# Kernel tuning notes

Hardware: AMD Instinct MI355X
Metric: run time of the kernel (lower is better)

## Reference

```python
import jax, jax.numpy as jnp
import numpy as np
import math

B, CK, T, H, W = 4, 64, 8, 30, 54
N, CV = 8, 512

def setup_inputs() -> dict:
    key = jax.random.key(0)
    k1, k2, k3, k4 = jax.random.split(key, 4)
    mem_keys = jax.random.normal(k1, (B, CK, T, H, W), dtype=jnp.float32)
    mem_values = jax.random.normal(k2, (N, CV, T, H, W), dtype=jnp.float32)
    qk = jax.random.normal(k3, (B, CK, H, W), dtype=jnp.float32)
    broadcast_map = jax.random.randint(k4, (N,), 0, B, dtype=jnp.int64)
    return {"mem_keys": mem_keys, "mem_values": mem_values, "qk": qk,
            "broadcast_map": broadcast_map}

def reference(mem_keys, mem_values, qk, broadcast_map):
    # STCNModel.read_memory
    Bq, CKq, Tq, Hq, Wq = mem_keys.shape
    mk = mem_keys.reshape(Bq, CKq, Tq * Hq * Wq)      # [B, CK, THW]
    q = qk.reshape(Bq, CKq, Hq * Wq)                   # [B, CK, HW]
    a_sq = jnp.sum(mk * mk, axis=1)[:, :, None]        # [B, THW, 1]
    ab = jnp.einsum('bct,bcq->btq', mk, q)             # [B, THW, HW]
    frame_affinity = (2.0 * ab - a_sq) / math.sqrt(CKq)
    # softmax over memory dim (axis=1)
    frame_affinity = jax.nn.softmax(frame_affinity, axis=1)
    obj_affinity = frame_affinity[broadcast_map]       # [N, THW, HW]
    Nn, CVv = mem_values.shape[0], mem_values.shape[1]
    mo = mem_values.reshape(Nn, CVv, Tq * Hq * Wq)     # [N, CV, THW]
    obj_read = jnp.einsum('nct,ntq->ncq', mo, obj_affinity)
    return obj_read.reshape(Nn, CVv, Hq, Wq)
```

## Files before the change

kernel.cpp:

```cpp
#include <hip/hip_runtime.h>
#include <hip/hip_bf16.h>

#define CKDIM 64
#define THW   12960
#define HWDIM 1620
#define NOBJ  8
#define CVAL  512
#define NB    4
#define NSTEP 405
#define NJT   13
#define NCHS  8
#define NCHP  4
#define PCH   16
#define S2F   0.3606737602222409f

using bf16x8 = __attribute__((ext_vector_type(8))) short;
using f32x4  = __attribute__((ext_vector_type(4))) float;

__device__ __forceinline__ unsigned cvtpk(float lo, float hi) {
    unsigned r;
    asm("v_cvt_pk_bf16_f32 %0, %1, %2" : "=v"(r) : "v"(lo), "v"(hi));
    return r;
}
__device__ __forceinline__ unsigned short bf_rne(float x) {
    unsigned u = __float_as_uint(x);
    u += 0x7FFFu + ((u >> 16) & 1u);
    return (unsigned short)(u >> 16);
}
__device__ __forceinline__ float fexp2(float x) {
#if __has_builtin(__builtin_amdgcn_exp2f)
    return __builtin_amdgcn_exp2f(x);
#else
    return __expf(x * 0.69314718055994531f);
#endif
}

__global__ void stcn_ksq_kernel(const float* __restrict__ mk, float* __restrict__ k8l) {
    int t = blockIdx.x * 256 + threadIdx.x;
    if (t >= THW) return;
    int b = blockIdx.y;
    const float* p = mk + (size_t)b * CKDIM * THW + t;
    float s = 0.f;
#pragma unroll
    for (int c = 0; c < CKDIM; ++c) { float v = p[(size_t)c * THW]; s = fmaf(v, v, s); }
    k8l[b * THW + t] = s * (0.125f * 1.44269504088896341f);
}

__global__ __launch_bounds__(512)
void stcn_ktr_kernel(const float* __restrict__ mk, unsigned short* __restrict__ kbt) {
    __shared__ unsigned short L[64][72];
    const int tid = threadIdx.x, b = blockIdx.y, t0 = blockIdx.x * 64;
#pragma unroll
    for (int it = 0; it < 8; ++it) {
        int idx = tid + 512 * it;
        int tt = idx & 63, c = idx >> 6;
        int t = t0 + tt;
        float v = (t < THW) ? mk[((size_t)b * CKDIM + c) * THW + t] : 0.f;
        L[tt][c] = bf_rne(v);
    }
    __syncthreads();
    int tt = tid >> 3, cq = tid & 7;
    int t = t0 + tt;
    if (t < THW) {
        uint4 o = *(const uint4*)&L[tt][8 * cq];
        *(uint4*)(kbt + ((size_t)b * THW + t) * CKDIM + 8 * cq) = o;
    }
}

__global__ void stcn_vcvt_kernel(const float* __restrict__ mv, unsigned short* __restrict__ mvb) {
    size_t i = ((size_t)blockIdx.x * 256 + threadIdx.x) * 8;
    if (i >= (size_t)NOBJ * CVAL * THW) return;
    float4 v0 = *(const float4*)(mv + i);
    float4 v1 = *(const float4*)(mv + i + 4);
    uint4 o;
    o.x = cvtpk(v0.x, v0.y); o.y = cvtpk(v0.z, v0.w);
    o.z = cvtpk(v1.x, v1.y); o.w = cvtpk(v1.z, v1.w);
    *(uint4*)(mvb + i) = o;
}

template <int MODE, bool VB16, bool KB16>
__global__ __launch_bounds__(512, (MODE == 1) ? 4 : 1)
void stcn_aff_kernel(const float* __restrict__ mk, const unsigned short* __restrict__ kbt,
                     const float* __restrict__ qk, const float* __restrict__ k8l,
                     float* __restrict__ mpart, float* __restrict__ lpart,
                     const float* __restrict__ mv, const unsigned short* __restrict__ mvb,
                     const int* __restrict__ bmap, float* __restrict__ out)
{
    constexpr int SMEM_BYTES = (MODE == 0) ? 36864 : 45312;
    __shared__ __align__(16) unsigned char smem[SMEM_BYTES];
    unsigned short* KtP   = (unsigned short*)smem;
    float*          k8tP  = (float*)(smem + 9216);
    unsigned short* PtP   = (unsigned short*)(smem + 9472);
    unsigned short* VtP   = (unsigned short*)(smem + 23808);
    float*          mjsP  = (float*)(smem + 44288);
    float*          iljsP = (float*)(smem + 44800);
    unsigned short* QtP   = (unsigned short*)smem;

    const int tid  = threadIdx.x;
    const int w    = tid >> 6;
    const int lane = tid & 63;
    const int g    = lane >> 4;
    const int lr   = lane & 15;

    int b, n = 0, jt, kc, cb = 0;
    if (MODE == 0) { b = blockIdx.y; jt = blockIdx.x >> 3; kc = blockIdx.x & 7; }
    else {
        n = blockIdx.y; jt = blockIdx.x >> 3; kc = (blockIdx.x >> 1) & 3; cb = blockIdx.x & 1;
        b = bmap[n];
    }
    const int jbase = jt * 128;
    const int cbase = cb * 256;

#pragma unroll
    for (int it = 0; it < 8; ++it) {
        int idx = tid + 512 * it;
        int j = idx & 127, cp = idx >> 7;
        int jg = jbase + j;
        float q0 = 0.f, q1 = 0.f;
        if (jg < HWDIM) {
            const float* qp = qk + ((size_t)b * CKDIM + 2 * cp) * HWDIM + jg;
            q0 = qp[0]; q1 = qp[HWDIM];
        }
        unsigned wh = cvtpk(q0, q1);
        float r0 = q0 - __uint_as_float(wh << 16);
        float r1 = q1 - __uint_as_float(wh & 0xFFFF0000u);
        *(unsigned*)&QtP[(0 * 128 + j) * 72 + 2 * cp] = wh;
        *(unsigned*)&QtP[(1 * 128 + j) * 72 + 2 * cp] = cvtpk(r0, r1);
    }
    __syncthreads();
    bf16x8 bqh[2], bql[2];
#pragma unroll
    for (int s = 0; s < 2; ++s) {
        bqh[s] = *(const bf16x8*)&QtP[(0 * 128 + w * 16 + lr) * 72 + 32 * s + 8 * g];
        bql[s] = *(const bf16x8*)&QtP[(1 * 128 + w * 16 + lr) * 72 + 32 * s + 8 * g];
    }
    __syncthreads();

    auto stageK_loads = [&](int st, uint2& k16, float2* kvf) {
        if constexpr (KB16) {
            int tt = tid >> 4, cq = tid & 15;
            k16 = *(const uint2*)(kbt + ((size_t)b * THW + st * 32 + tt) * CKDIM + 4 * cq);
        } else {
#pragma unroll
            for (int it = 0; it < 2; ++it) {
                int idx = tid + 512 * it;
                int tt = idx & 31, cp = idx >> 5;
                const float* kp = mk + ((size_t)b * CKDIM + 2 * cp) * THW + st * 32 + tt;
                kvf[it].x = kp[0];
                kvf[it].y = kp[THW];
            }
        }
    };
    auto stageK_write = [&](int buf, uint2 k16, const float2* kvf) {
        if constexpr (KB16) {
            int tt = tid >> 4, cq = tid & 15;
            *(uint2*)&KtP[(buf * 32 + tt) * 72 + 4 * cq] = k16;
        } else {
#pragma unroll
            for (int it = 0; it < 2; ++it) {
                int idx = tid + 512 * it;
                int tt = idx & 31, cp = idx >> 5;
                *(unsigned*)&KtP[(buf * 32 + tt) * 72 + 2 * cp] = cvtpk(kvf[it].x, kvf[it].y);
            }
        }
    };

    int s0, s1;
    if (MODE == 0) { s0 = (NSTEP * kc) / NCHS; s1 = (NSTEP * (kc + 1)) / NCHS; }
    else           { s0 = (NSTEP * kc) / NCHP; s1 = (NSTEP * (kc + 1)) / NCHP; }

    if (MODE == 1 && tid < 128) {
        int jg = jbase + tid;
        float m = 0.f, l = 0.f;
        if (jg < HWDIM) {
            m = -1e30f;
#pragma unroll
            for (int c = 0; c < NCHS; ++c) {
                float mc = mpart[(b * NCHS + c) * HWDIM + jg];
                float lc = lpart[(b * NCHS + c) * HWDIM + jg];
                float mn = fmaxf(m, mc);
                l = l * fexp2(m - mn) + lc * fexp2(mc - mn);
                m = mn;
            }
        }
        mjsP[tid]  = m;
        iljsP[tid] = (l > 0.f) ? 1.f / l : 0.f;
    }
    {
        uint2 k16; float2 kvf[2];
        stageK_loads(s0, k16, kvf);
        stageK_write(0, k16, kvf);
        if (tid < 32) k8tP[tid] = k8l[b * THW + s0 * 32 + tid];
    }
    __syncthreads();

    float mv_j = 0.f, il_j = 0.f;
    if (MODE == 1) { mv_j = mjsP[w * 16 + lr]; il_j = iljsP[w * 16 + lr]; }

    float m_run = -1e30f, l_run = 0.f;
    f32x4 zz = {0.f, 0.f, 0.f, 0.f};
    f32x4 acc[4][4];
    if (MODE == 1)
#pragma unroll
        for (int i = 0; i < 4; ++i)
#pragma unroll
            for (int j = 0; j < 4; ++j) acc[i][j] = zz;

    const int wc = w >> 1, wj = w & 1;
    const int vc = tid >> 1, vth = tid & 1;

    int cur = 0;
    for (int st = s0; st < s1; ++st) {
        const int t0 = st * 32;
        const bool nxt = (st + 1 < s1);

        uint4 vw0 = {0,0,0,0}, vw1 = {0,0,0,0};
        if (MODE == 1) {
            if (VB16) {
                const unsigned short* vp = mvb + ((size_t)n * CVAL + cbase + vc) * THW + t0 + vth * 16;
                vw0 = *(const uint4*)vp;
                vw1 = *(const uint4*)(vp + 8);
            } else {
                const float* vp = mv + ((size_t)n * CVAL + cbase + vc) * THW + t0 + vth * 16;
                float4 f0 = *(const float4*)vp;
                float4 f1 = *(const float4*)(vp + 4);
                float4 f2 = *(const float4*)(vp + 8);
                float4 f3 = *(const float4*)(vp + 12);
                vw0 = make_uint4(cvtpk(f0.x,f0.y), cvtpk(f0.z,f0.w), cvtpk(f1.x,f1.y), cvtpk(f1.z,f1.w));
                vw1 = make_uint4(cvtpk(f2.x,f2.y), cvtpk(f2.z,f2.w), cvtpk(f3.x,f3.y), cvtpk(f3.z,f3.w));
            }
        }
        uint2 k16; float2 kvf[2];
        float k8next = 0.f;
        if (nxt) {
            stageK_loads(st + 1, k16, kvf);
            if (tid < 32) k8next = k8l[b * THW + (st + 1) * 32 + tid];
        }
        bf16x8 ak0[2], ak1[2];
#pragma unroll
        for (int s = 0; s < 2; ++s) {
            ak0[s] = *(const bf16x8*)&KtP[(cur * 32 + lr) * 72 + 32 * s + 8 * g];
            ak1[s] = *(const bf16x8*)&KtP[(cur * 32 + 16 + lr) * 72 + 32 * s + 8 * g];
        }
        f32x4 k80 = *(const f32x4*)&k8tP[cur * 32 + 4 * g];
        f32x4 k81 = *(const f32x4*)&k8tP[cur * 32 + 16 + 4 * g];
        f32x4 ab0 = zz, ab1 = zz;
#pragma unroll
        for (int s = 0; s < 2; ++s) {
            ab0 = __builtin_amdgcn_mfma_f32_16x16x32_bf16(ak0[s], bqh[s], ab0, 0, 0, 0);
            ab0 = __builtin_amdgcn_mfma_f32_16x16x32_bf16(ak0[s], bql[s], ab0, 0, 0, 0);
            ab1 = __builtin_amdgcn_mfma_f32_16x16x32_bf16(ak1[s], bqh[s], ab1, 0, 0, 0);
            ab1 = __builtin_amdgcn_mfma_f32_16x16x32_bf16(ak1[s], bql[s], ab1, 0, 0, 0);
        }
        if (nxt) {
            stageK_write(cur ^ 1, k16, kvf);
            if (tid < 32) k8tP[(cur ^ 1) * 32 + tid] = k8next;
        }

        if (MODE == 0) {
            float L0[4], L1[4], tmax = -1e30f;
#pragma unroll
            for (int r = 0; r < 4; ++r) {
                L0[r] = fmaf(ab0[r], S2F, -k80[r]); tmax = fmaxf(tmax, L0[r]);
                L1[r] = fmaf(ab1[r], S2F, -k81[r]); tmax = fmaxf(tmax, L1[r]);
            }
            float ps = 0.f;
#pragma unroll
            for (int r = 0; r < 4; ++r)
                ps += fexp2(L0[r] - tmax) + fexp2(L1[r] - tmax);
            float mn = fmaxf(m_run, tmax);
            l_run = l_run * fexp2(m_run - mn) + ps * fexp2(tmax - mn);
            m_run = mn;
            __syncthreads();
        } else {
            float p0[4], p1[4];
#pragma unroll
            for (int r = 0; r < 4; ++r) {
                p0[r] = fexp2(fmaf(ab0[r], S2F, -k80[r]) - mv_j) * il_j;
                p1[r] = fexp2(fmaf(ab1[r], S2F, -k81[r]) - mv_j) * il_j;
            }
            __syncthreads();
            {
                int jl = w * 16 + lr;
                *(uint2*)&PtP[jl * 56 + 4 * g]      = make_uint2(cvtpk(p0[0], p0[1]), cvtpk(p0[2], p0[3]));
                *(uint2*)&PtP[jl * 56 + 16 + 4 * g] = make_uint2(cvtpk(p1[0], p1[1]), cvtpk(p1[2], p1[3]));
                *(uint4*)&VtP[vc * 40 + vth * 16]     = vw0;
                *(uint4*)&VtP[vc * 40 + vth * 16 + 8] = vw1;
            }
            __syncthreads();
            bf16x8 bp[4];
#pragma unroll
            for (int jf = 0; jf < 4; ++jf)
                bp[jf] = *(const bf16x8*)&PtP[(wj * 64 + jf * 16 + lr) * 56 + 8 * g];
#pragma unroll
            for (int cf = 0; cf < 4; ++cf) {
                bf16x8 av = *(const bf16x8*)&VtP[(wc * 64 + cf * 16 + lr) * 40 + 8 * g];
#pragma unroll
                for (int jf = 0; jf < 4; ++jf)
                    acc[cf][jf] = __builtin_amdgcn_mfma_f32_16x16x32_bf16(av, bp[jf], acc[cf][jf], 0, 0, 0);
            }
        }
        cur ^= 1;
    }

    if (MODE == 0) {
#pragma unroll
        for (int off = 16; off < 64; off <<= 1) {
            float mo = __shfl_xor(m_run, off, 64);
            float lo = __shfl_xor(l_run, off, 64);
            float mn = fmaxf(m_run, mo);
            l_run = l_run * fexp2(m_run - mn) + lo * fexp2(mo - mn);
            m_run = mn;
        }
        int jg = jbase + w * 16 + lr;
        if (g == 0 && jg < HWDIM) {
            mpart[(b * NCHS + kc) * HWDIM + jg] = m_run;
            lpart[(b * NCHS + kc) * HWDIM + jg] = l_run;
        }
    } else {
#pragma unroll
        for (int cf = 0; cf < 4; ++cf) {
#pragma unroll
            for (int jf = 0; jf < 4; ++jf) {
                int jg = jbase + wj * 64 + jf * 16 + lr;
                if (jg < HWDIM) {
                    int c = cbase + wc * 64 + cf * 16 + 4 * g;
                    float* op = out + ((size_t)n * CVAL + c) * HWDIM + jg;
#pragma unroll
                    for (int r = 0; r < 4; ++r)
                        atomicAdd(op + (size_t)r * HWDIM, acc[cf][jf][r]);
                }
            }
        }
    }
}

__global__ __launch_bounds__(512)
void stcn_pwrite_kernel(const unsigned short* __restrict__ kbt,
                        const float* __restrict__ qk, const float* __restrict__ k8l,
                        const float* __restrict__ mpart, const float* __restrict__ lpart,
                        unsigned short* __restrict__ Pws, int bbase)
{
    __shared__ __align__(16) unsigned char smem[36864];
    unsigned short* KtP   = (unsigned short*)smem;
    float*          k8tP  = (float*)(smem + 9216);
    unsigned short* PtP   = (unsigned short*)(smem + 9472);
    float*          mjsP  = (float*)(smem + 23808);
    float*          iljsP = (float*)(smem + 24320);
    unsigned short* QtP   = (unsigned short*)smem;

    const int tid  = threadIdx.x;
    const int w    = tid >> 6;
    const int lane = tid & 63;
    const int g    = lane >> 4;
    const int lr   = lane & 15;

    const int bb = blockIdx.y;
    const int b  = bbase + bb;
    const int jt = blockIdx.x >> 4, kc = blockIdx.x & 15;
    const int jbase = jt * 128;

#pragma unroll
    for (int it = 0; it < 8; ++it) {
        int idx = tid + 512 * it;
        int j = idx & 127, cp = idx >> 7;
        int jg = jbase + j;
        float q0 = 0.f, q1 = 0.f;
        if (jg < HWDIM) {
            const float* qp = qk + ((size_t)b * CKDIM + 2 * cp) * HWDIM + jg;
            q0 = qp[0]; q1 = qp[HWDIM];
        }
        unsigned wh = cvtpk(q0, q1);
        float r0 = q0 - __uint_as_float(wh << 16);
        float r1 = q1 - __uint_as_float(wh & 0xFFFF0000u);
        *(unsigned*)&QtP[(0 * 128 + j) * 72 + 2 * cp] = wh;
        *(unsigned*)&QtP[(1 * 128 + j) * 72 + 2 * cp] = cvtpk(r0, r1);
    }
    __syncthreads();
    bf16x8 bqh[2], bql[2];
#pragma unroll
    for (int s = 0; s < 2; ++s) {
        bqh[s] = *(const bf16x8*)&QtP[(0 * 128 + w * 16 + lr) * 72 + 32 * s + 8 * g];
        bql[s] = *(const bf16x8*)&QtP[(1 * 128 + w * 16 + lr) * 72 + 32 * s + 8 * g];
    }
    __syncthreads();

    const int s0 = (NSTEP * kc) / PCH, s1 = (NSTEP * (kc + 1)) / PCH;

    if (tid < 128) {
        int jg = jbase + tid;
        float m = 0.f, l = 0.f;
        if (jg < HWDIM) {
            m = -1e30f;
#pragma unroll
            for (int c = 0; c < NCHS; ++c) {
                float mc = mpart[(b * NCHS + c) * HWDIM + jg];
                float lc = lpart[(b * NCHS + c) * HWDIM + jg];
                float mn = fmaxf(m, mc);
                l = l * fexp2(m - mn) + lc * fexp2(mc - mn);
                m = mn;
            }
        }
        mjsP[tid]  = m;
        iljsP[tid] = (l > 0.f) ? 1.f / l : 0.f;
    }
    {
        int tt = tid >> 4, cq = tid & 15;
        uint2 k16 = *(const uint2*)(kbt + ((size_t)b * THW + s0 * 32 + tt) * CKDIM + 4 * cq);
        *(uint2*)&KtP[tt * 72 + 4 * cq] = k16;
        if (tid < 32) k8tP[tid] = k8l[b * THW + s0 * 32 + tid];
    }
    __syncthreads();

    const float mv_j = mjsP[w * 16 + lr], il_j = iljsP[w * 16 + lr];
    f32x4 zz = {0.f, 0.f, 0.f, 0.f};

    int cur = 0;
    for (int st = s0; st < s1; ++st) {
        const int t0 = st * 32;
        const bool nxt = (st + 1 < s1);
        uint2 k16;
        float k8next = 0.f;
        const int tt = tid >> 4, cq = tid & 15;
        if (nxt) {
            k16 = *(const uint2*)(kbt + ((size_t)b * THW + (st + 1) * 32 + tt) * CKDIM + 4 * cq);
            if (tid < 32) k8next = k8l[b * THW + (st + 1) * 32 + tid];
        }
        bf16x8 ak0[2], ak1[2];
#pragma unroll
        for (int s = 0; s < 2; ++s) {
            ak0[s] = *(const bf16x8*)&KtP[(cur * 32 + lr) * 72 + 32 * s + 8 * g];
            ak1[s] = *(const bf16x8*)&KtP[(cur * 32 + 16 + lr) * 72 + 32 * s + 8 * g];
        }
        f32x4 k80 = *(const f32x4*)&k8tP[cur * 32 + 4 * g];
        f32x4 k81 = *(const f32x4*)&k8tP[cur * 32 + 16 + 4 * g];
        f32x4 ab0 = zz, ab1 = zz;
#pragma unroll
        for (int s = 0; s < 2; ++s) {
            ab0 = __builtin_amdgcn_mfma_f32_16x16x32_bf16(ak0[s], bqh[s], ab0, 0, 0, 0);
            ab0 = __builtin_amdgcn_mfma_f32_16x16x32_bf16(ak0[s], bql[s], ab0, 0, 0, 0);
            ab1 = __builtin_amdgcn_mfma_f32_16x16x32_bf16(ak1[s], bqh[s], ab1, 0, 0, 0);
            ab1 = __builtin_amdgcn_mfma_f32_16x16x32_bf16(ak1[s], bql[s], ab1, 0, 0, 0);
        }
        if (nxt) {
            *(uint2*)&KtP[((cur ^ 1) * 32 + tt) * 72 + 4 * cq] = k16;
            if (tid < 32) k8tP[(cur ^ 1) * 32 + tid] = k8next;
        }
        float p0[4], p1[4];
#pragma unroll
        for (int r = 0; r < 4; ++r) {
            p0[r] = fexp2(fmaf(ab0[r], S2F, -k80[r]) - mv_j) * il_j;
            p1[r] = fexp2(fmaf(ab1[r], S2F, -k81[r]) - mv_j) * il_j;
        }
        __syncthreads();
        {
            int jl = w * 16 + lr;
            *(uint2*)&PtP[jl * 56 + 4 * g]      = make_uint2(cvtpk(p0[0], p0[1]), cvtpk(p0[2], p0[3]));
            *(uint2*)&PtP[jl * 56 + 16 + 4 * g] = make_uint2(cvtpk(p1[0], p1[1]), cvtpk(p1[2], p1[3]));
        }
        __syncthreads();
        {
            int jr = tid >> 2, qq = tid & 3;
            int jg = jbase + jr;
            if (jg < HWDIM)
                *(uint4*)(Pws + ((size_t)bb * HWDIM + jg) * THW + t0 + qq * 8) =
                    *(const uint4*)&PtP[jr * 56 + qq * 8];
        }
        cur ^= 1;
    }
}

template <bool FULLP>
__global__ __launch_bounds__(512, 4)
void stcn_gemm2_kernel(const unsigned short* __restrict__ mvb,
                       const unsigned short* __restrict__ Pws,
                       const int* __restrict__ bmap, float* __restrict__ out, int phase)
{
    __shared__ __align__(16) unsigned short Av[2][256 * 40];
    __shared__ __align__(16) unsigned short Bv[2][128 * 40];

    const int n = blockIdx.y;
    const int b = bmap[n];
    int bslot;
    if constexpr (FULLP) { bslot = b; }
    else { if ((b >> 1) != phase) return; bslot = b & 1; }

    const int x    = blockIdx.x;
    const int ks   = x & 3;
    const int rest = x >> 2;
    const int jn   = rest % NJT;
    const int cm   = rest / NJT;
    const int jbase = jn * 128, cbase = cm * 256;

    const int tid = threadIdx.x, w = tid >> 6, lane = tid & 63, g = lane >> 4, lr = lane & 15;
    const int wc = w >> 1, wj = w & 1;

    const int arow = tid >> 1, at = (tid & 1) * 16;
    const int brow = tid >> 2, bt = (tid & 3) * 8;
    const unsigned short* vsrc = mvb + ((size_t)n * CVAL + cbase + arow) * THW + at;
    const int jrow = jbase + brow;
    const bool jok = jrow < HWDIM;
    const unsigned short* psrc = Pws + ((size_t)bslot * HWDIM + (jok ? jrow : 0)) * THW + bt;

    const int s0 = (NSTEP * ks) / 4, s1 = (NSTEP * (ks + 1)) / 4;

    f32x4 zz = {0.f, 0.f, 0.f, 0.f};
    f32x4 acc[4][4];
#pragma unroll
    for (int i = 0; i < 4; ++i)
#pragma unroll
        for (int j = 0; j < 4; ++j) acc[i][j] = zz;

    const uint4 zq = make_uint4(0, 0, 0, 0);
    {
        uint4 ta0 = *(const uint4*)(vsrc + (size_t)s0 * 32);
        uint4 ta1 = *(const uint4*)(vsrc + (size_t)s0 * 32 + 8);
        uint4 tb0 = jok ? *(const uint4*)(psrc + (size_t)s0 * 32) : zq;
        *(uint4*)&Av[0][arow * 40 + at]     = ta0;
        *(uint4*)&Av[0][arow * 40 + at + 8] = ta1;
        *(uint4*)&Bv[0][brow * 40 + bt]     = tb0;
    }
    uint4 nA0 = *(const uint4*)(vsrc + (size_t)(s0 + 1) * 32);
    uint4 nA1 = *(const uint4*)(vsrc + (size_t)(s0 + 1) * 32 + 8);
    uint4 nB0 = jok ? *(const uint4*)(psrc + (size_t)(s0 + 1) * 32) : zq;
    __syncthreads();

    int cur = 0;
    for (int st = s0; st < s1; ++st) {
        const bool h1 = (st + 1 < s1), h2 = (st + 2 < s1);
        uint4 fA0, fA1, fB0;
        if (h2) {
            fA0 = *(const uint4*)(vsrc + (size_t)(st + 2) * 32);
            fA1 = *(const uint4*)(vsrc + (size_t)(st + 2) * 32 + 8);
            fB0 = jok ? *(const uint4*)(psrc + (size_t)(st + 2) * 32) : zq;
        }
        bf16x8 bp[4];
#pragma unroll
        for (int jf = 0; jf < 4; ++jf)
            bp[jf] = *(const bf16x8*)&Bv[cur][(wj * 64 + jf * 16 + lr) * 40 + 8 * g];
        if (h1) {
            *(uint4*)&Av[cur ^ 1][arow * 40 + at]     = nA0;
            *(uint4*)&Av[cur ^ 1][arow * 40 + at + 8] = nA1;
            *(uint4*)&Bv[cur ^ 1][brow * 40 + bt]     = nB0;
        }
#pragma unroll
        for (int cf = 0; cf < 4; ++cf) {
            bf16x8 av = *(const bf16x8*)&Av[cur][(wc * 64 + cf * 16 + lr) * 40 + 8 * g];
#pragma unroll
            for (int jf = 0; jf < 4; ++jf)
                acc[cf][jf] = __builtin_amdgcn_mfma_f32_16x16x32_bf16(av, bp[jf], acc[cf][jf], 0, 0, 0);
        }
        __syncthreads();
        if (h2) { nA0 = fA0; nA1 = fA1; nB0 = fB0; }
        cur ^= 1;
    }

#pragma unroll
    for (int cf = 0; cf < 4; ++cf)
#pragma unroll
        for (int jf = 0; jf < 4; ++jf) {
            int jg = jbase + wj * 64 + jf * 16 + lr;
            if (jg < HWDIM) {
                int c = cbase + wc * 64 + cf * 16 + 4 * g;
                float* op = out + ((size_t)n * CVAL + c) * HWDIM + jg;
#pragma unroll
                for (int r = 0; r < 4; ++r)
                    atomicAdd(op + (size_t)r * HWDIM, acc[cf][jf][r]);
            }
        }
}

extern "C" void kernel_launch(void* const* d_in, const int* in_sizes, int n_in,
                              void* d_out, int out_size, void* d_ws, size_t ws_size,
                              hipStream_t stream) {
    (void)in_sizes; (void)n_in;
    const float* mk   = (const float*)d_in[0];
    const float* mv   = (const float*)d_in[1];
    const float* qkp  = (const float*)d_in[2];
    const int*   bmap = (const int*)d_in[3];
    float* out = (float*)d_out;

    float* k8l   = (float*)d_ws;
    float* mpart = k8l + NB * THW;
    float* lpart = mpart + NB * NCHS * HWDIM;
    unsigned short* mvb = (unsigned short*)(lpart + NB * NCHS * HWDIM);
    unsigned short* kbt = mvb + (size_t)NOBJ * CVAL * THW;
    unsigned short* Pws = kbt + (size_t)NB * THW * CKDIM;

    size_t base_bytes = (size_t)(NB * THW + 2 * NB * NCHS * HWDIM) * 4;
    size_t need_vb  = base_bytes + (size_t)NOBJ * CVAL * THW * 2;
    size_t need_kbt = need_vb + (size_t)NB * THW * CKDIM * 2;
    size_t need_P2  = need_kbt + (size_t)2 * HWDIM * THW * 2;
    size_t need_P4  = need_kbt + (size_t)4 * HWDIM * THW * 2;
    bool use_vb16 = (ws_size >= need_vb);
    bool use_kbt  = (ws_size >= need_kbt);
    bool use_P2   = (ws_size >= need_P2);
    bool use_P4   = (ws_size >= need_P4);

    hipMemsetAsync(d_out, 0, (size_t)out_size * sizeof(float), stream);
    stcn_ksq_kernel<<<dim3((THW + 255) / 256, NB), 256, 0, stream>>>(mk, k8l);
    if (use_kbt)
        stcn_ktr_kernel<<<dim3((THW + 63) / 64, NB), 512, 0, stream>>>(mk, kbt);
    if (use_vb16) {
        size_t nthreads = (size_t)NOBJ * CVAL * THW / 8;
        stcn_vcvt_kernel<<<(unsigned)((nthreads + 255) / 256), 256, 0, stream>>>(mv, mvb);
    }

    if (use_kbt)
        stcn_aff_kernel<0, false, true><<<dim3(NJT * NCHS, NB), 512, 0, stream>>>(
            mk, kbt, qkp, k8l, mpart, lpart, nullptr, nullptr, nullptr, nullptr);
    else
        stcn_aff_kernel<0, false, false><<<dim3(NJT * NCHS, NB), 512, 0, stream>>>(
            mk, nullptr, qkp, k8l, mpart, lpart, nullptr, nullptr, nullptr, nullptr);

    if (use_P4 && use_kbt) {
        stcn_pwrite_kernel<<<dim3(NJT * PCH, NB), 512, 0, stream>>>(
            kbt, qkp, k8l, mpart, lpart, Pws, 0);
        stcn_gemm2_kernel<true><<<dim3(104, NOBJ), 512, 0, stream>>>(
            mvb, Pws, bmap, out, 0);
    } else if (use_P2 && use_kbt) {
        for (int p = 0; p < 2; ++p) {
            stcn_pwrite_kernel<<<dim3(NJT * PCH, 2), 512, 0, stream>>>(
                kbt, qkp, k8l, mpart, lpart, Pws, 2 * p);
            stcn_gemm2_kernel<false><<<dim3(104, NOBJ), 512, 0, stream>>>(
                mvb, Pws, bmap, out, p);
        }
    } else {
        dim3 g1(NJT * NCHP * 2, NOBJ);
        if (use_vb16 && use_kbt)
            stcn_aff_kernel<1, true, true><<<g1, 512, 0, stream>>>(
                mk, kbt, qkp, k8l, mpart, lpart, nullptr, mvb, bmap, out);
        else if (use_vb16)
            stcn_aff_kernel<1, true, false><<<g1, 512, 0, stream>>>(
                mk, nullptr, qkp, k8l, mpart, lpart, nullptr, mvb, bmap, out);
        else
            stcn_aff_kernel<1, false, false><<<g1, 512, 0, stream>>>(
                mk, nullptr, qkp, k8l, mpart, lpart, mv, nullptr, bmap, out);
    }
}
```

Before: 554.1 us.

## Rewrite value-GEMM with direct global-to-LDS loads, swizzled LDS and 128x128 tiles

Replaces the 512-thread, 256x128-tile value GEMM with a 256-thread, 128x128-tile version that uses half the K-split (2 instead of 4) while keeping the same grid size. Operand tiles are staged with global_load_lds (async copies straight into LDS, when the builtin is available) into XOR-swizzled unpadded LDS buffers, removing the register round-trip and padding. Out-of-range j rows now read row 0 instead of zeros, which only affects discarded output columns. The change trades fewer atomic partial sums and less LDS for smaller per-block reuse and a shallower prefetch pipeline.

```diff
diff --git a/kernel.cpp b/kernel.cpp
--- a/kernel.cpp
+++ b/kernel.cpp
@@ -14,6 +14,12 @@
 #define PCH   16
 #define S2F   0.3606737602222409f
 
+#if defined(__has_builtin)
+#if __has_builtin(__builtin_amdgcn_global_load_lds)
+#define HAVE_GLL 1
+#endif
+#endif
+
 using bf16x8 = __attribute__((ext_vector_type(8))) short;
 using f32x4  = __attribute__((ext_vector_type(4))) float;
 
@@ -34,6 +40,13 @@
     return __expf(x * 0.69314718055994531f);
 #endif
 }
+#ifdef HAVE_GLL
+__device__ __forceinline__ void gload16(const void* g, void* l) {
+    __builtin_amdgcn_global_load_lds(
+        (const __attribute__((address_space(1))) unsigned int*)g,
+        (__attribute__((address_space(3))) unsigned int*)l, 16, 0, 0);
+}
+#endif
 
 __global__ void stcn_ksq_kernel(const float* __restrict__ mk, float* __restrict__ k8l) {
     int t = blockIdx.x * 256 + threadIdx.x;
@@ -471,13 +484,13 @@
 }
 
 template <bool FULLP>
-__global__ __launch_bounds__(512, 4)
-void stcn_gemm2_kernel(const unsigned short* __restrict__ mvb,
+__global__ __launch_bounds__(256, 4)
+void stcn_gemm3_kernel(const unsigned short* __restrict__ mvb,
                        const unsigned short* __restrict__ Pws,
                        const int* __restrict__ bmap, float* __restrict__ out, int phase)
 {
-    __shared__ __align__(16) unsigned short Av[2][256 * 40];
-    __shared__ __align__(16) unsigned short Bv[2][128 * 40];
+    __shared__ __align__(16) unsigned short Av[2][128 * 32];
+    __shared__ __align__(16) unsigned short Bv[2][128 * 32];
 
     const int n = blockIdx.y;
     const int b = bmap[n];
@@ -486,23 +499,30 @@
     else { if ((b >> 1) != phase) return; bslot = b & 1; }
 
     const int x    = blockIdx.x;
-    const int ks   = x & 3;
-    const int rest = x >> 2;
+    const int ks   = x & 1;
+    const int rest = x >> 1;
     const int jn   = rest % NJT;
     const int cm   = rest / NJT;
-    const int jbase = jn * 128, cbase = cm * 256;
-
-    const int tid = threadIdx.x, w = tid >> 6, lane = tid & 63, g = lane >> 4, lr = lane & 15;
+    const int jbase = jn * 128, cbase = cm * 128;
+
+    const int tid = threadIdx.x;
+    const int w = tid >> 6, lane = tid & 63, g = lane >> 4, lr = lane & 15;
     const int wc = w >> 1, wj = w & 1;
 
-    const int arow = tid >> 1, at = (tid & 1) * 16;
-    const int brow = tid >> 2, bt = (tid & 3) * 8;
-    const unsigned short* vsrc = mvb + ((size_t)n * CVAL + cbase + arow) * THW + at;
-    const int jrow = jbase + brow;
-    const bool jok = jrow < HWDIM;
-    const unsigned short* psrc = Pws + ((size_t)bslot * HWDIM + (jok ? jrow : 0)) * THW + bt;
-
-    const int s0 = (NSTEP * ks) / 4, s1 = (NSTEP * (ks + 1)) / 4;
+    const int srow = tid >> 2;
+    const int tsw  = (((tid & 3) ^ ((tid >> 3) & 3)) << 3);
+    const int gs8  = ((g ^ ((lr >> 1) & 3)) << 3);
+
+    const int s0 = (NSTEP * ks) / 2, s1 = (NSTEP * (ks + 1)) / 2;
+
+    const unsigned short* abase = mvb + ((size_t)n * CVAL + cbase) * THW;
+    const unsigned short* bbase = Pws + (size_t)bslot * HWDIM * THW;
+    int jr0 = jbase + srow;       if (jr0 >= HWDIM) jr0 = 0;
+    int jr1 = jbase + 64 + srow;  if (jr1 >= HWDIM) jr1 = 0;
+    const unsigned short* ga0 = abase + (size_t)(srow) * THW + tsw;
+    const unsigned short* ga1 = abase + (size_t)(64 + srow) * THW + tsw;
+    const unsigned short* gb0 = bbase + (size_t)jr0 * THW + tsw;
+    const unsigned short* gb1 = bbase + (size_t)jr1 * THW + tsw;
 
     f32x4 zz = {0.f, 0.f, 0.f, 0.f};
     f32x4 acc[4][4];
@@ -511,47 +531,62 @@
 #pragma unroll
         for (int j = 0; j < 4; ++j) acc[i][j] = zz;
 
-    const uint4 zq = make_uint4(0, 0, 0, 0);
+#ifdef HAVE_GLL
+    auto stage = [&](int buf, int st) {
+        const int t0 = st * 32;
+        gload16(ga0 + t0, &Av[buf][0    + w * 512]);
+        gload16(ga1 + t0, &Av[buf][2048 + w * 512]);
+        gload16(gb0 + t0, &Bv[buf][0    + w * 512]);
+        gload16(gb1 + t0, &Bv[buf][2048 + w * 512]);
+    };
+    stage(0, s0);
+#else
     {
-        uint4 ta0 = *(const uint4*)(vsrc + (size_t)s0 * 32);
-        uint4 ta1 = *(const uint4*)(vsrc + (size_t)s0 * 32 + 8);
-        uint4 tb0 = jok ? *(const uint4*)(psrc + (size_t)s0 * 32) : zq;
-        *(uint4*)&Av[0][arow * 40 + at]     = ta0;
-        *(uint4*)&Av[0][arow * 40 + at + 8] = ta1;
-        *(uint4*)&Bv[0][brow * 40 + bt]     = tb0;
-    }
-    uint4 nA0 = *(const uint4*)(vsrc + (size_t)(s0 + 1) * 32);
-    uint4 nA1 = *(const uint4*)(vsrc + (size_t)(s0 + 1) * 32 + 8);
-    uint4 nB0 = jok ? *(const uint4*)(psrc + (size_t)(s0 + 1) * 32) : zq;
+        const int t0 = s0 * 32;
+        *(uint4*)&Av[0][tid * 8]        = *(const uint4*)(ga0 + t0);
+        *(uint4*)&Av[0][2048 + tid * 8] = *(const uint4*)(ga1 + t0);
+        *(uint4*)&Bv[0][tid * 8]        = *(const uint4*)(gb0 + t0);
+        *(uint4*)&Bv[0][2048 + tid * 8] = *(const uint4*)(gb1 + t0);
+    }
+#endif
     __syncthreads();
 
     int cur = 0;
     for (int st = s0; st < s1; ++st) {
-        const bool h1 = (st + 1 < s1), h2 = (st + 2 < s1);
-        uint4 fA0, fA1, fB0;
-        if (h2) {
-            fA0 = *(const uint4*)(vsrc + (size_t)(st + 2) * 32);
-            fA1 = *(const uint4*)(vsrc + (size_t)(st + 2) * 32 + 8);
-            fB0 = jok ? *(const uint4*)(psrc + (size_t)(st + 2) * 32) : zq;
-        }
-        bf16x8 bp[4];
+        const bool nxt = (st + 1 < s1);
+#ifdef HAVE_GLL
+        if (nxt) stage(cur ^ 1, st + 1);
+#else
+        uint4 ra0, ra1, rb0, rb1;
+        if (nxt) {
+            const int t0 = (st + 1) * 32;
+            ra0 = *(const uint4*)(ga0 + t0);
+            ra1 = *(const uint4*)(ga1 + t0);
+            rb0 = *(const uint4*)(gb0 + t0);
+            rb1 = *(const uint4*)(gb1 + t0);
+        }
+#endif
+        bf16x8 av[4], bp[4];
+#pragma unroll
+        for (int cf = 0; cf < 4; ++cf)
+            av[cf] = *(const bf16x8*)&Av[cur][(wc * 64 + cf * 16 + lr) * 32 + gs8];
 #pragma unroll
         for (int jf = 0; jf < 4; ++jf)
-            bp[jf] = *(const bf16x8*)&Bv[cur][(wj * 64 + jf * 16 + lr) * 40 + 8 * g];
-        if (h1) {
-            *(uint4*)&Av[cur ^ 1][arow * 40 + at]     = nA0;
-            *(uint4*)&Av[cur ^ 1][arow * 40 + at + 8] = nA1;
-            *(uint4*)&Bv[cur ^ 1][brow * 40 + bt]     = nB0;
-        }
-#pragma unroll
-        for (int cf = 0; cf < 4; ++cf) {
-            bf16x8 av = *(const bf16x8*)&Av[cur][(wc * 64 + cf * 16 + lr) * 40 + 8 * g];
+            bp[jf] = *(const bf16x8*)&Bv[cur][(wj * 64 + jf * 16 + lr) * 32 + gs8];
+#pragma unroll
+        for (int cf = 0; cf < 4; ++cf)
 #pragma unroll
             for (int jf = 0; jf < 4; ++jf)
-                acc[cf][jf] = __builtin_amdgcn_mfma_f32_16x16x32_bf16(av, bp[jf], acc[cf][jf], 0, 0, 0);
-        }
+                acc[cf][jf] = __builtin_amdgcn_mfma_f32_16x16x32_bf16(av[cf], bp[jf], acc[cf][jf], 0, 0, 0);
+#ifndef HAVE_GLL
+        if (nxt) {
+            *(uint4*)&Av[cur ^ 1][tid * 8]        = ra0;
+            *(uint4*)&Av[cur ^ 1][2048 + tid * 8] = ra1;
+            *(uint4*)&Bv[cur ^ 1][tid * 8]        = rb0;
+            *(uint4*)&Bv[cur ^ 1][2048 + tid * 8] = rb1;
+        }
+#endif
         __syncthreads();
-        if (h2) { nA0 = fA0; nA1 = fA1; nB0 = fB0; }
         cur ^= 1;
     }
 
@@ -616,13 +651,13 @@
     if (use_P4 && use_kbt) {
         stcn_pwrite_kernel<<<dim3(NJT * PCH, NB), 512, 0, stream>>>(
             kbt, qkp, k8l, mpart, lpart, Pws, 0);
-        stcn_gemm2_kernel<true><<<dim3(104, NOBJ), 512, 0, stream>>>(
+        stcn_gemm3_kernel<true><<<dim3(104, NOBJ), 256, 0, stream>>>(
             mvb, Pws, bmap, out, 0);
     } else if (use_P2 && use_kbt) {
         for (int p = 0; p < 2; ++p) {
             stcn_pwrite_kernel<<<dim3(NJT * PCH, 2), 512, 0, stream>>>(
                 kbt, qkp, k8l, mpart, lpart, Pws, 2 * p);
-            stcn_gemm2_kernel<false><<<dim3(104, NOBJ), 512, 0, stream>>>(
+            stcn_gemm3_kernel<false><<<dim3(104, NOBJ), 256, 0, stream>>>(
                 mvb, Pws, bmap, out, p);
         }
     } else {
```

Measured after the change: 553.2 us. Within noise of the previous version (-0.2%).
